# Kernel optimization log

Measured on AMD Instinct MI355X. Metric: run time of the kernel, lower is better.

Reference implementation:

```python
import jax, jax.numpy as jnp
import numpy as np

MARGIN = 0.3
EPS = 1e-12


def setup_inputs() -> dict:
    key = jax.random.key(0)
    k1, k2, k3, k4 = jax.random.split(key, 4)
    B, N, D = 4, 6400, 32
    pred_masks = jax.random.normal(k1, (B, N, D), dtype=jnp.float32)
    pos_rand = jax.random.uniform(k2, (B, N), dtype=jnp.float32)
    target_gt_idx = jax.random.randint(k3, (B, N), 0, 20, dtype=jnp.int64)
    fg_mask = jax.random.randint(k4, (B, N), 0, 2) > 0
    return {
        "pred_masks": pred_masks,
        "pos_rand": pos_rand,
        "target_gt_idx": target_gt_idx,
        "fg_mask": fg_mask,
    }


def reference(pred_masks, pos_rand, target_gt_idx, fg_mask):
    B, N, D = pred_masks.shape
    # L2-normalize coefficients (F.normalize, eps=1e-12)
    norm = jnp.sqrt(jnp.sum(pred_masks * pred_masks, axis=-1, keepdims=True))
    coeffs = pred_masks / jnp.maximum(norm, EPS)  # [B,N,D]

    valid_pair = fg_mask[:, :, None] & fg_mask[:, None, :]  # [B,N,N]
    same_inst = target_gt_idx[:, :, None] == target_gt_idx[:, None, :]
    eye = jnp.eye(N, dtype=bool)
    S = valid_pair & same_inst & ~eye          # positives (same instance, not self)
    Dm = valid_pair & ~same_inst               # negatives (different instance)

    # Cosine similarities (vectors are unit norm)
    sims = jnp.einsum('bnd,bmd->bnm', coeffs, coeffs)  # [B,N,N]

    # Hardest negative per anchor: argmax similarity among negatives
    neg_idx = jnp.argmax(jnp.where(Dm, sims, -jnp.inf), axis=-1)  # [B,N]
    neg_vec = jnp.take_along_axis(coeffs, neg_idx[..., None], axis=1)  # [B,N,D]

    # Random positive: pick the k-th positive in anchor order, k = floor(u*num_pos)
    num_pos = jnp.sum(S, axis=-1)  # [B,N]
    pos_choice = jnp.floor(pos_rand * num_pos.astype(pos_rand.dtype)).astype(jnp.int32)
    pos_choice = jnp.clip(pos_choice, 0, jnp.maximum(num_pos - 1, 0).astype(jnp.int32))
    cum = jnp.cumsum(S.astype(jnp.int32), axis=-1)  # rank of each positive
    sel = S & (cum == (pos_choice + 1)[..., None])  # one-hot over chosen positive
    pos_idx = jnp.argmax(sel, axis=-1)  # [B,N]
    pos_vec = jnp.take_along_axis(coeffs, pos_idx[..., None], axis=1)  # [B,N,D]

    pos_d = jnp.sqrt(jnp.sum((coeffs - pos_vec) ** 2, axis=-1) + EPS)
    neg_d = jnp.sqrt(jnp.sum((coeffs - neg_vec) ** 2, axis=-1) + EPS)

    valid = fg_mask & (num_pos >= 1) & jnp.any(Dm, axis=-1)  # anchor forms a triplet
    per_anchor = jnp.maximum(pos_d - neg_d + MARGIN, 0.0)
    n_trip = jnp.sum(valid)
    total = jnp.sum(per_anchor * valid.astype(per_anchor.dtype))
    return jnp.where(n_trip > 0, total / jnp.maximum(n_trip, 1).astype(total.dtype), 0.0)
```

## Files before the change

### kernel.cpp

```cpp
#include <hip/hip_runtime.h>
#include <math.h>

#define B_ 4
#define N_ 6400
#define D_ 32
#define TJ 256
#define TI 128
#define CHUNK 256
#define NCC 25
#define NCLS 20
#define CSROW 24
#define TOTB (NCC * B_)
#define NPASS 650

typedef __attribute__((ext_vector_type(4))) float f32x4;
typedef __attribute__((ext_vector_type(8))) short bf16x8;

static constexpr float MARGIN_ = 0.3f;

__device__ __forceinline__ unsigned fmap(float f) {
    unsigned u = __float_as_uint(f);
    return (u & 0x80000000u) ? ~u : (u | 0x80000000u);
}
__device__ __forceinline__ float funmap(unsigned u) {
    return (u & 0x80000000u) ? __uint_as_float(u ^ 0x80000000u)
                             : __uint_as_float(~u);
}
#define NEG_INF_MAPPED 0x007FFFFFu

__device__ __forceinline__ unsigned short f2bf(float f) {
    unsigned u = __float_as_uint(f);
    unsigned r = u + 0x7fffu + ((u >> 16) & 1u);
    return (unsigned short)(r >> 16);
}
__device__ __forceinline__ float bf2f(unsigned short h) {
    return __uint_as_float(((unsigned)h) << 16);
}
__device__ __forceinline__ void bf2x(unsigned u, float& e0, float& e1) {
    e0 = __uint_as_float(u << 16);
    e1 = __uint_as_float(u & 0xffff0000u);
}
__device__ __forceinline__ float dpair(unsigned xh, unsigned xl, unsigned yh, unsigned yl) {
    float a0, a1, b0, b1, c0, c1, d0, d1;
    bf2x(xh, a0, a1); bf2x(xl, b0, b1);
    bf2x(yh, c0, c1); bf2x(yl, d0, d1);
    return fmaf(a0 + b0, c0 + d0, (a1 + b1) * (c1 + d1));
}

__global__ __launch_bounds__(256) void k_prep(const float* __restrict__ pred,
                                              const int* __restrict__ gt,
                                              const int* __restrict__ fg,
                                              unsigned short* __restrict__ hi_g,
                                              unsigned short* __restrict__ lo_g,
                                              int* __restrict__ clist,
                                              int* __restrict__ cgS,
                                              int* __restrict__ Marr,
                                              int* __restrict__ csArr,
                                              unsigned* __restrict__ bestArr,
                                              unsigned* __restrict__ done) {
    int c = blockIdx.x, b = blockIdx.y;
    int t = threadIdx.x, lane = t & 63, w = t >> 6;
    int idx = c * CHUNK + t;

    bestArr[b * N_ + idx] = NEG_INF_MAPPED;
    if (c == 0 && b == 0 && t == 0) *done = 0u;

    __shared__ int cntL[NCC * NCLS];
    __shared__ int wv[4 * NCLS];
    __shared__ int totL[NCLS];
    __shared__ int csL[NCLS + 1];
    for (int k = t; k < NCC * NCLS; k += 256) cntL[k] = 0;
    __syncthreads();

    for (int cc = w; cc < NCC; cc += 4) {
        const int4 f4 = ((const int4*)(fg + (size_t)b * N_ + cc * CHUNK))[lane];
        const int4 g4 = ((const int4*)(gt + (size_t)b * N_ + cc * CHUNK))[lane];
        if (f4.x) atomicAdd(&cntL[cc * NCLS + g4.x], 1);
        if (f4.y) atomicAdd(&cntL[cc * NCLS + g4.y], 1);
        if (f4.z) atomicAdd(&cntL[cc * NCLS + g4.z], 1);
        if (f4.w) atomicAdd(&cntL[cc * NCLS + g4.w], 1);
    }

    bool flag = fg[b * N_ + idx] != 0;
    int cls = flag ? gt[b * N_ + idx] : 0;
    int rnk = 0;
    unsigned long long below = (1ull << lane) - 1ull;
    for (int k = 0; k < NCLS; ++k) {
        unsigned long long m = __ballot(flag && (cls == k));
        if (flag && cls == k) rnk = __popcll(m & below);
        if (lane == 0) wv[w * NCLS + k] = __popcll(m);
    }
    __syncthreads();

    if (t < NCLS) {
        int s = 0;
        #pragma unroll
        for (int cc = 0; cc < NCC; ++cc) s += cntL[cc * NCLS + t];
        totL[t] = s;
    }
    __syncthreads();
    if (t <= NCLS) {
        int s = 0;
        for (int k = 0; k < t; ++k) s += totL[k];
        csL[t] = s;
    }
    __syncthreads();
    if (c == 0) {
        if (t == 0) Marr[b] = csL[NCLS];
        if (t <= NCLS) csArr[b * CSROW + t] = csL[t];
    }
    if (!flag) return;

    int pre = 0;
    for (int cc = 0; cc < c; ++cc) pre += cntL[cc * NCLS + cls];
    int woff = 0;
    #pragma unroll
    for (int k = 0; k < 4; ++k) if (k < w) woff += wv[k * NCLS + cls];
    int dest = csL[cls] + pre + woff + rnk;
    clist[b * N_ + dest] = idx;
    cgS[b * N_ + dest] = cls;

    const float4* s4 = (const float4*)(pred + ((size_t)b * N_ + idx) * D_);
    float f[32];
    float ssq = 0.0f;
    #pragma unroll
    for (int k = 0; k < 8; ++k) {
        float4 q = s4[k];
        f[k * 4] = q.x; f[k * 4 + 1] = q.y; f[k * 4 + 2] = q.z; f[k * 4 + 3] = q.w;
        ssq += q.x * q.x + q.y * q.y + q.z * q.z + q.w * q.w;
    }
    float inv = 1.0f / fmaxf(sqrtf(ssq), 1e-12f);
    unsigned hw[16], lw[16];
    #pragma unroll
    for (int k = 0; k < 16; ++k) {
        float x0 = f[2 * k] * inv, x1 = f[2 * k + 1] * inv;
        unsigned short h0 = f2bf(x0), h1 = f2bf(x1);
        unsigned short l0 = f2bf(x0 - bf2f(h0)), l1 = f2bf(x1 - bf2f(h1));
        hw[k] = (unsigned)h0 | ((unsigned)h1 << 16);
        lw[k] = (unsigned)l0 | ((unsigned)l1 << 16);
    }
    uint4* dh = (uint4*)(hi_g + ((size_t)b * N_ + dest) * 32);
    uint4* dl = (uint4*)(lo_g + ((size_t)b * N_ + dest) * 32);
    #pragma unroll
    for (int k = 0; k < 4; ++k) {
        dh[k] = make_uint4(hw[4 * k], hw[4 * k + 1], hw[4 * k + 2], hw[4 * k + 3]);
        dl[k] = make_uint4(lw[4 * k], lw[4 * k + 1], lw[4 * k + 2], lw[4 * k + 3]);
    }
}

__global__ __launch_bounds__(256) void k_pass(const unsigned short* __restrict__ hi_g,
                                              const unsigned short* __restrict__ lo_g,
                                              const int* __restrict__ cgS,
                                              const int* __restrict__ Marr,
                                              const int* __restrict__ csArr,
                                              unsigned* __restrict__ bestArr) {
    int b = blockIdx.y;
    int M = Marr[b];
    int f = blockIdx.x;
    int bj = (int)((sqrtf(4.0f * (float)f + 1.0f) - 1.0f) * 0.5f);
    if ((bj + 1) * (bj + 2) <= f) ++bj;
    if (bj * (bj + 1) > f) --bj;
    int bi = f - bj * (bj + 1);
    int i0 = bi * TI;
    int j0 = bj * TJ;
    if (i0 >= M || j0 >= M) return;

    __shared__ __align__(16) unsigned short sc_hi[TJ * 40];
    __shared__ __align__(16) unsigned short sc_lo[TJ * 40];
    __shared__ int sg[TJ];
    __shared__ float colb[4 * TJ];
    int t = threadIdx.x;

    {
        int j = j0 + t;
        sg[t] = (j < M) ? cgS[b * N_ + j] : -1;
        #pragma unroll
        for (int k = 0; k < 4; ++k) colb[k * 256 + t] = -INFINITY;
    }
    {
        int seg = t & 3, r0 = t >> 2;
        #pragma unroll
        for (int p = 0; p < 4; ++p) {
            int row = p * 64 + r0;
            int j = j0 + row;
            uint4 vh = make_uint4(0u, 0u, 0u, 0u), vl = make_uint4(0u, 0u, 0u, 0u);
            if (j < M) {
                vh = *(const uint4*)(hi_g + ((size_t)b * N_ + j) * 32 + seg * 8);
                vl = *(const uint4*)(lo_g + ((size_t)b * N_ + j) * 32 + seg * 8);
            }
            *(uint4*)(sc_hi + row * 40 + seg * 8) = vh;
            *(uint4*)(sc_lo + row * 40 + seg * 8) = vl;
        }
    }
    __syncthreads();

    int lane = t & 63, w = t >> 6;
    int r = lane & 15, quad = lane >> 4;
    int ib = i0 + w * 32;

    if (ib < M) {
        bf16x8 a_hi[2], a_lo[2];
        int gt_i[2][4];
        #pragma unroll
        for (int it = 0; it < 2; ++it) {
            int i = ib + it * 16 + r;
            bf16x8 zh = {0, 0, 0, 0, 0, 0, 0, 0};
            a_hi[it] = zh; a_lo[it] = zh;
            if (i < M) {
                a_hi[it] = *(const bf16x8*)(hi_g + ((size_t)b * N_ + i) * 32 + quad * 8);
                a_lo[it] = *(const bf16x8*)(lo_g + ((size_t)b * N_ + i) * 32 + quad * 8);
            }
            #pragma unroll
            for (int r4 = 0; r4 < 4; ++r4) {
                int ia = ib + it * 16 + quad * 4 + r4;
                gt_i[it][r4] = (ia < M) ? cgS[b * N_ + ia] : -2;
            }
        }

        int ilast = min(ib + 31, M - 1);
        int cmin = cgS[b * N_ + ib];
        int cmax = cgS[b * N_ + ilast];
        int posLo = csArr[b * CSROW + cmin];
        int posHi = csArr[b * CSROW + cmax + 1];
        bool oneCls = (cmin == cmax);

        float best[2][4];
        #pragma unroll
        for (int it = 0; it < 2; ++it)
            #pragma unroll
            for (int r4 = 0; r4 < 4; ++r4) best[it][r4] = -INFINITY;

        int jrows = min(TJ, M - j0);
        int ntile = (jrows + 15) >> 4;
        for (int jt = 0; jt < ntile; ++jt) {
            int jlo = j0 + jt * 16;
            int jvhi = min(jlo + 16, j0 + jrows);
            if (oneCls && jlo >= posLo && jvhi <= posHi) continue;

            bf16x8 bh = *(const bf16x8*)(sc_hi + (jt * 16 + r) * 40 + quad * 8);
            bf16x8 bl = *(const bf16x8*)(sc_lo + (jt * 16 + r) * 40 + quad * 8);
            bool full = (jt * 16 + 16) <= jrows;
            float cb = -INFINITY;

            if (full && (jlo + 16 <= posLo || jlo >= posHi)) {
                #pragma unroll
                for (int it = 0; it < 2; ++it) {
                    f32x4 acc = {0.f, 0.f, 0.f, 0.f};
                    acc = __builtin_amdgcn_mfma_f32_16x16x32_bf16(a_hi[it], bh, acc, 0, 0, 0);
                    acc = __builtin_amdgcn_mfma_f32_16x16x32_bf16(a_hi[it], bl, acc, 0, 0, 0);
                    acc = __builtin_amdgcn_mfma_f32_16x16x32_bf16(a_lo[it], bh, acc, 0, 0, 0);
                    #pragma unroll
                    for (int r4 = 0; r4 < 4; ++r4) {
                        float v = acc[r4];
                        best[it][r4] = fmaxf(best[it][r4], v);
                        cb = fmaxf(cb, (gt_i[it][r4] >= 0) ? v : -INFINITY);
                    }
                }
            } else {
                int gtj = sg[jt * 16 + r];
                bool jv = (gtj >= 0);
                #pragma unroll
                for (int it = 0; it < 2; ++it) {
                    f32x4 acc = {0.f, 0.f, 0.f, 0.f};
                    acc = __builtin_amdgcn_mfma_f32_16x16x32_bf16(a_hi[it], bh, acc, 0, 0, 0);
                    acc = __builtin_amdgcn_mfma_f32_16x16x32_bf16(a_hi[it], bl, acc, 0, 0, 0);
                    acc = __builtin_amdgcn_mfma_f32_16x16x32_bf16(a_lo[it], bh, acc, 0, 0, 0);
                    #pragma unroll
                    for (int r4 = 0; r4 < 4; ++r4) {
                        bool same = (gtj == gt_i[it][r4]);
                        float sm = (same || !jv) ? -INFINITY : acc[r4];
                        best[it][r4] = fmaxf(best[it][r4], sm);
                        cb = fmaxf(cb, (gt_i[it][r4] >= 0) ? sm : -INFINITY);
                    }
                }
            }

            cb = fmaxf(cb, __shfl_xor(cb, 16));
            cb = fmaxf(cb, __shfl_xor(cb, 32));
            if (lane < 16) colb[w * TJ + jt * 16 + lane] = cb;
        }

        #pragma unroll
        for (int it = 0; it < 2; ++it) {
            #pragma unroll
            for (int r4 = 0; r4 < 4; ++r4) {
                float bb = best[it][r4];
                #pragma unroll
                for (int mk = 1; mk < 16; mk <<= 1)
                    bb = fmaxf(bb, __shfl_xor(bb, mk));
                if (r == 0) {
                    int ia = ib + it * 16 + quad * 4 + r4;
                    if (ia < M && bb > -INFINITY)
                        atomicMax(&bestArr[b * N_ + ia], fmap(bb));
                }
            }
        }
    }

    __syncthreads();
    {
        float v = fmaxf(fmaxf(colb[t], colb[TJ + t]),
                        fmaxf(colb[2 * TJ + t], colb[3 * TJ + t]));
        int j = j0 + t;
        if (j < M && v > -INFINITY)
            atomicMax(&bestArr[b * N_ + j], fmap(v));
    }
}

__global__ __launch_bounds__(256) void k_combine(const unsigned short* __restrict__ hi_g,
                                                 const unsigned short* __restrict__ lo_g,
                                                 const int* __restrict__ cgS,
                                                 const int* __restrict__ clist,
                                                 const int* __restrict__ Marr,
                                                 const int* __restrict__ csArr,
                                                 const float* __restrict__ pos_rand,
                                                 const unsigned* __restrict__ bestArr,
                                                 unsigned* __restrict__ partS,
                                                 unsigned* __restrict__ partC,
                                                 unsigned* __restrict__ done,
                                                 float* __restrict__ out) {
    int b = blockIdx.y;
    int M = Marr[b];
    int t = threadIdx.x, lane = t & 63, w = t >> 6;
    int i = blockIdx.x * 256 + t;

    float contrib = 0.0f;
    int vflag = 0;
    if (i < M) {
        int cls = cgS[b * N_ + i];
        int s0 = csArr[b * CSROW + cls];
        int s1 = csArr[b * CSROW + cls + 1];
        int num_pos = s1 - s0 - 1;
        unsigned bu = bestArr[b * N_ + i];
        if (num_pos >= 1 && bu != NEG_INF_MAPPED) {
            float best = funmap(bu);
            int orig = clist[b * N_ + i];
            float u = pos_rand[b * N_ + orig];
            int pcx = (int)floorf(u * (float)num_pos);
            int hi2 = num_pos - 1;
            pcx = pcx < 0 ? 0 : (pcx > hi2 ? hi2 : pcx);
            int ri = i - s0;
            int posj = s0 + pcx + (pcx >= ri ? 1 : 0);

            const uint4* xh4 = (const uint4*)(hi_g + ((size_t)b * N_ + i) * 32);
            const uint4* xl4 = (const uint4*)(lo_g + ((size_t)b * N_ + i) * 32);
            const uint4* yh4 = (const uint4*)(hi_g + ((size_t)b * N_ + posj) * 32);
            const uint4* yl4 = (const uint4*)(lo_g + ((size_t)b * N_ + posj) * 32);
            float dot = 0.0f;
            #pragma unroll
            for (int q = 0; q < 4; ++q) {
                uint4 XH = xh4[q], XL = xl4[q], YH = yh4[q], YL = yl4[q];
                dot += dpair(XH.x, XL.x, YH.x, YL.x);
                dot += dpair(XH.y, XL.y, YH.y, YL.y);
                dot += dpair(XH.z, XL.z, YH.z, YL.z);
                dot += dpair(XH.w, XL.w, YH.w, YL.w);
            }
            float pos_d = sqrtf(fmaxf(2.f - 2.f * dot, 0.f) + 1e-12f);
            float neg_d = sqrtf(fmaxf(2.f - 2.f * best, 0.f) + 1e-12f);
            contrib = fmaxf(pos_d - neg_d + MARGIN_, 0.0f);
            vflag = 1;
        }
    }

    #pragma unroll
    for (int off = 32; off > 0; off >>= 1) {
        contrib += __shfl_down(contrib, off);
        vflag += __shfl_down(vflag, off);
    }
    __shared__ float ssum[4];
    __shared__ int scnt[4];
    if (lane == 0) { ssum[w] = contrib; scnt[w] = vflag; }
    __syncthreads();

    if (w == 0) {
        int bid = b * NCC + blockIdx.x;
        int last = 0;
        if (lane == 0) {
            float bs = ssum[0] + ssum[1] + ssum[2] + ssum[3];
            int bc = scnt[0] + scnt[1] + scnt[2] + scnt[3];
            atomicExch(&partS[bid], __float_as_uint(bs));
            atomicExch(&partC[bid], (unsigned)bc);
            __threadfence();
            last = (atomicAdd(done, 1u) == (unsigned)(TOTB - 1)) ? 1 : 0;
        }
        last = __shfl(last, 0);
        if (last) {
            float T = 0.0f; int C = 0;
            for (int k = lane; k < TOTB; k += 64) {
                T += __uint_as_float(atomicAdd(&partS[k], 0u));
                C += (int)atomicAdd(&partC[k], 0u);
            }
            #pragma unroll
            for (int off = 32; off > 0; off >>= 1) {
                T += __shfl_down(T, off);
                C += __shfl_down(C, off);
            }
            if (lane == 0) out[0] = (C > 0) ? (T / (float)C) : 0.0f;
        }
    }
}

extern "C" void kernel_launch(void* const* d_in, const int* in_sizes, int n_in,
                              void* d_out, int out_size, void* d_ws, size_t ws_size,
                              hipStream_t stream) {
    const float* pred     = (const float*)d_in[0];
    const float* pos_rand = (const float*)d_in[1];
    const int*   gt       = (const int*)d_in[2];
    const int*   fg       = (const int*)d_in[3];
    float* out = (float*)d_out;

    char* ws = (char*)d_ws;
    unsigned short* hi_g    = (unsigned short*)(ws);
    unsigned short* lo_g    = (unsigned short*)(ws + 1638400);
    int*            clist   = (int*)(ws + 3276800);
    int*            cgS     = (int*)(ws + 3379200);
    int*            Marr    = (int*)(ws + 3481600);
    int*            csArr   = (int*)(ws + 3481664);
    unsigned*       done    = (unsigned*)(ws + 3482048);
    unsigned*       partS   = (unsigned*)(ws + 3482112);
    unsigned*       partC   = (unsigned*)(ws + 3482624);
    unsigned*       bestArr = (unsigned*)(ws + 3483136);

    dim3 gpr(NCC, B_);
    k_prep<<<gpr, 256, 0, stream>>>(pred, gt, fg, hi_g, lo_g, clist, cgS, Marr, csArr, bestArr, done);
    dim3 gp(NPASS, B_);
    k_pass<<<gp, 256, 0, stream>>>(hi_g, lo_g, cgS, Marr, csArr, bestArr);
    dim3 gc(NCC, B_);
    k_combine<<<gc, 256, 0, stream>>>(hi_g, lo_g, cgS, clist, Marr, csArr, pos_rand, bestArr, partS, partC, done, out);
}
```

Before: 93.84 us.

## Fuse combine stage into pass kernel via last-block-per-batch completion counter

Removes the separate k_combine launch. Each k_pass block bumps a per-batch counter when it finishes, and the last block for each batch runs the per-anchor loss over all M anchors in a single 256-thread block, then does a cross-batch final reduction through a second counter. It also adds an all-valid fast path in the off-diagonal MFMA tile that drops the per-row validity select. This saves one launch and its gap, at the cost of a serial tail where one block per batch handles up to 6400 anchors.

```diff
diff --git a/kernel.cpp b/kernel.cpp
--- a/kernel.cpp
+++ b/kernel.cpp
@@ -10,7 +10,6 @@
 #define NCC 25
 #define NCLS 20
 #define CSROW 24
-#define TOTB (NCC * B_)
 #define NPASS 650
 
 typedef __attribute__((ext_vector_type(4))) float f32x4;
@@ -57,13 +56,15 @@
                                               int* __restrict__ Marr,
                                               int* __restrict__ csArr,
                                               unsigned* __restrict__ bestArr,
-                                              unsigned* __restrict__ done) {
+                                              unsigned* __restrict__ passDone,
+                                              unsigned* __restrict__ combDone) {
     int c = blockIdx.x, b = blockIdx.y;
     int t = threadIdx.x, lane = t & 63, w = t >> 6;
     int idx = c * CHUNK + t;
 
     bestArr[b * N_ + idx] = NEG_INF_MAPPED;
-    if (c == 0 && b == 0 && t == 0) *done = 0u;
+    if (c == 0 && t == 0) passDone[b] = 0u;
+    if (c == 0 && b == 0 && t == 0) *combDone = 0u;
 
     __shared__ int cntL[NCC * NCLS];
     __shared__ int wv[4 * NCLS];
@@ -151,9 +152,16 @@
 __global__ __launch_bounds__(256) void k_pass(const unsigned short* __restrict__ hi_g,
                                               const unsigned short* __restrict__ lo_g,
                                               const int* __restrict__ cgS,
+                                              const int* __restrict__ clist,
                                               const int* __restrict__ Marr,
                                               const int* __restrict__ csArr,
-                                              unsigned* __restrict__ bestArr) {
+                                              const float* __restrict__ pos_rand,
+                                              unsigned* __restrict__ bestArr,
+                                              unsigned* __restrict__ passDone,
+                                              unsigned* __restrict__ combDone,
+                                              unsigned* __restrict__ partS,
+                                              unsigned* __restrict__ partC,
+                                              float* __restrict__ out) {
     int b = blockIdx.y;
     int M = Marr[b];
     int f = blockIdx.x;
@@ -163,239 +171,241 @@
     int bi = f - bj * (bj + 1);
     int i0 = bi * TI;
     int j0 = bj * TJ;
-    if (i0 >= M || j0 >= M) return;
+    int t = threadIdx.x;
+    int lane = t & 63, w = t >> 6;
 
     __shared__ __align__(16) unsigned short sc_hi[TJ * 40];
     __shared__ __align__(16) unsigned short sc_lo[TJ * 40];
     __shared__ int sg[TJ];
     __shared__ float colb[4 * TJ];
-    int t = threadIdx.x;
-
-    {
-        int j = j0 + t;
-        sg[t] = (j < M) ? cgS[b * N_ + j] : -1;
-        #pragma unroll
-        for (int k = 0; k < 4; ++k) colb[k * 256 + t] = -INFINITY;
-    }
-    {
-        int seg = t & 3, r0 = t >> 2;
-        #pragma unroll
-        for (int p = 0; p < 4; ++p) {
-            int row = p * 64 + r0;
-            int j = j0 + row;
-            uint4 vh = make_uint4(0u, 0u, 0u, 0u), vl = make_uint4(0u, 0u, 0u, 0u);
-            if (j < M) {
-                vh = *(const uint4*)(hi_g + ((size_t)b * N_ + j) * 32 + seg * 8);
-                vl = *(const uint4*)(lo_g + ((size_t)b * N_ + j) * 32 + seg * 8);
-            }
-            *(uint4*)(sc_hi + row * 40 + seg * 8) = vh;
-            *(uint4*)(sc_lo + row * 40 + seg * 8) = vl;
-        }
-    }
-    __syncthreads();
-
-    int lane = t & 63, w = t >> 6;
-    int r = lane & 15, quad = lane >> 4;
-    int ib = i0 + w * 32;
-
-    if (ib < M) {
-        bf16x8 a_hi[2], a_lo[2];
-        int gt_i[2][4];
-        #pragma unroll
-        for (int it = 0; it < 2; ++it) {
-            int i = ib + it * 16 + r;
-            bf16x8 zh = {0, 0, 0, 0, 0, 0, 0, 0};
-            a_hi[it] = zh; a_lo[it] = zh;
-            if (i < M) {
-                a_hi[it] = *(const bf16x8*)(hi_g + ((size_t)b * N_ + i) * 32 + quad * 8);
-                a_lo[it] = *(const bf16x8*)(lo_g + ((size_t)b * N_ + i) * 32 + quad * 8);
-            }
-            #pragma unroll
-            for (int r4 = 0; r4 < 4; ++r4) {
-                int ia = ib + it * 16 + quad * 4 + r4;
-                gt_i[it][r4] = (ia < M) ? cgS[b * N_ + ia] : -2;
-            }
-        }
-
-        int ilast = min(ib + 31, M - 1);
-        int cmin = cgS[b * N_ + ib];
-        int cmax = cgS[b * N_ + ilast];
-        int posLo = csArr[b * CSROW + cmin];
-        int posHi = csArr[b * CSROW + cmax + 1];
-        bool oneCls = (cmin == cmax);
-
-        float best[2][4];
-        #pragma unroll
-        for (int it = 0; it < 2; ++it)
-            #pragma unroll
-            for (int r4 = 0; r4 < 4; ++r4) best[it][r4] = -INFINITY;
-
-        int jrows = min(TJ, M - j0);
-        int ntile = (jrows + 15) >> 4;
-        for (int jt = 0; jt < ntile; ++jt) {
-            int jlo = j0 + jt * 16;
-            int jvhi = min(jlo + 16, j0 + jrows);
-            if (oneCls && jlo >= posLo && jvhi <= posHi) continue;
-
-            bf16x8 bh = *(const bf16x8*)(sc_hi + (jt * 16 + r) * 40 + quad * 8);
-            bf16x8 bl = *(const bf16x8*)(sc_lo + (jt * 16 + r) * 40 + quad * 8);
-            bool full = (jt * 16 + 16) <= jrows;
-            float cb = -INFINITY;
-
-            if (full && (jlo + 16 <= posLo || jlo >= posHi)) {
+
+    bool activeBlk = (i0 < M) && (j0 < M);
+    if (activeBlk) {
+        {
+            int j = j0 + t;
+            sg[t] = (j < M) ? cgS[b * N_ + j] : -1;
+            #pragma unroll
+            for (int k = 0; k < 4; ++k) colb[k * 256 + t] = -INFINITY;
+        }
+        {
+            int seg = t & 3, r0 = t >> 2;
+            #pragma unroll
+            for (int p = 0; p < 4; ++p) {
+                int row = p * 64 + r0;
+                int j = j0 + row;
+                uint4 vh = make_uint4(0u, 0u, 0u, 0u), vl = make_uint4(0u, 0u, 0u, 0u);
+                if (j < M) {
+                    vh = *(const uint4*)(hi_g + ((size_t)b * N_ + j) * 32 + seg * 8);
+                    vl = *(const uint4*)(lo_g + ((size_t)b * N_ + j) * 32 + seg * 8);
+                }
+                *(uint4*)(sc_hi + row * 40 + seg * 8) = vh;
+                *(uint4*)(sc_lo + row * 40 + seg * 8) = vl;
+            }
+        }
+        __syncthreads();
+
+        int r = lane & 15, quad = lane >> 4;
+        int ib = i0 + w * 32;
+
+        if (ib < M) {
+            bf16x8 a_hi[2], a_lo[2];
+            int gt_i[2][4];
+            #pragma unroll
+            for (int it = 0; it < 2; ++it) {
+                int i = ib + it * 16 + r;
+                bf16x8 zh = {0, 0, 0, 0, 0, 0, 0, 0};
+                a_hi[it] = zh; a_lo[it] = zh;
+                if (i < M) {
+                    a_hi[it] = *(const bf16x8*)(hi_g + ((size_t)b * N_ + i) * 32 + quad * 8);
+                    a_lo[it] = *(const bf16x8*)(lo_g + ((size_t)b * N_ + i) * 32 + quad * 8);
+                }
                 #pragma unroll
-                for (int it = 0; it < 2; ++it) {
-                    f32x4 acc = {0.f, 0.f, 0.f, 0.f};
-                    acc = __builtin_amdgcn_mfma_f32_16x16x32_bf16(a_hi[it], bh, acc, 0, 0, 0);
-                    acc = __builtin_amdgcn_mfma_f32_16x16x32_bf16(a_hi[it], bl, acc, 0, 0, 0);
-                    acc = __builtin_amdgcn_mfma_f32_16x16x32_bf16(a_lo[it], bh, acc, 0, 0, 0);
+                for (int r4 = 0; r4 < 4; ++r4) {
+                    int ia = ib + it * 16 + quad * 4 + r4;
+                    gt_i[it][r4] = (ia < M) ? cgS[b * N_ + ia] : -2;
+                }
+            }
+
+            int ilast = min(ib + 31, M - 1);
+            int cmin = cgS[b * N_ + ib];
+            int cmax = cgS[b * N_ + ilast];
+            int posLo = csArr[b * CSROW + cmin];
+            int posHi = csArr[b * CSROW + cmax + 1];
+            bool oneCls = (cmin == cmax);
+            bool allValid = (ib + 31 < M);
+
+            float best[2][4];
+            #pragma unroll
+            for (int it = 0; it < 2; ++it)
+                #pragma unroll
+                for (int r4 = 0; r4 < 4; ++r4) best[it][r4] = -INFINITY;
+
+            int jrows = min(TJ, M - j0);
+            int ntile = (jrows + 15) >> 4;
+            for (int jt = 0; jt < ntile; ++jt) {
+                int jlo = j0 + jt * 16;
+                int jvhi = min(jlo + 16, j0 + jrows);
+                if (oneCls && jlo >= posLo && jvhi <= posHi) continue;
+
+                bf16x8 bh = *(const bf16x8*)(sc_hi + (jt * 16 + r) * 40 + quad * 8);
+                bf16x8 bl = *(const bf16x8*)(sc_lo + (jt * 16 + r) * 40 + quad * 8);
+                bool full = (jt * 16 + 16) <= jrows;
+                float cb = -INFINITY;
+
+                if (full && (jlo + 16 <= posLo || jlo >= posHi)) {
+                    if (allValid) {
+                        #pragma unroll
+                        for (int it = 0; it < 2; ++it) {
+                            f32x4 acc = {0.f, 0.f, 0.f, 0.f};
+                            acc = __builtin_amdgcn_mfma_f32_16x16x32_bf16(a_hi[it], bh, acc, 0, 0, 0);
+                            acc = __builtin_amdgcn_mfma_f32_16x16x32_bf16(a_hi[it], bl, acc, 0, 0, 0);
+                            acc = __builtin_amdgcn_mfma_f32_16x16x32_bf16(a_lo[it], bh, acc, 0, 0, 0);
+                            #pragma unroll
+                            for (int r4 = 0; r4 < 4; ++r4) {
+                                float v = acc[r4];
+                                best[it][r4] = fmaxf(best[it][r4], v);
+                                cb = fmaxf(cb, v);
+                            }
+                        }
+                    } else {
+                        #pragma unroll
+                        for (int it = 0; it < 2; ++it) {
+                            f32x4 acc = {0.f, 0.f, 0.f, 0.f};
+                            acc = __builtin_amdgcn_mfma_f32_16x16x32_bf16(a_hi[it], bh, acc, 0, 0, 0);
+                            acc = __builtin_amdgcn_mfma_f32_16x16x32_bf16(a_hi[it], bl, acc, 0, 0, 0);
+                            acc = __builtin_amdgcn_mfma_f32_16x16x32_bf16(a_lo[it], bh, acc, 0, 0, 0);
+                            #pragma unroll
+                            for (int r4 = 0; r4 < 4; ++r4) {
+                                float v = acc[r4];
+                                best[it][r4] = fmaxf(best[it][r4], v);
+                                cb = fmaxf(cb, (gt_i[it][r4] >= 0) ? v : -INFINITY);
+                            }
+                        }
+                    }
+                } else {
+                    int gtj = sg[jt * 16 + r];
+                    bool jv = (gtj >= 0);
                     #pragma unroll
-                    for (int r4 = 0; r4 < 4; ++r4) {
-                        float v = acc[r4];
-                        best[it][r4] = fmaxf(best[it][r4], v);
-                        cb = fmaxf(cb, (gt_i[it][r4] >= 0) ? v : -INFINITY);
+                    for (int it = 0; it < 2; ++it) {
+                        f32x4 acc = {0.f, 0.f, 0.f, 0.f};
+                        acc = __builtin_amdgcn_mfma_f32_16x16x32_bf16(a_hi[it], bh, acc, 0, 0, 0);
+                        acc = __builtin_amdgcn_mfma_f32_16x16x32_bf16(a_hi[it], bl, acc, 0, 0, 0);
+                        acc = __builtin_amdgcn_mfma_f32_16x16x32_bf16(a_lo[it], bh, acc, 0, 0, 0);
+                        #pragma unroll
+                        for (int r4 = 0; r4 < 4; ++r4) {
+                            bool same = (gtj == gt_i[it][r4]);
+                            float sm = (same || !jv) ? -INFINITY : acc[r4];
+                            best[it][r4] = fmaxf(best[it][r4], sm);
+                            cb = fmaxf(cb, (gt_i[it][r4] >= 0) ? sm : -INFINITY);
+                        }
                     }
                 }
-            } else {
-                int gtj = sg[jt * 16 + r];
-                bool jv = (gtj >= 0);
+
+                cb = fmaxf(cb, __shfl_xor(cb, 16));
+                cb = fmaxf(cb, __shfl_xor(cb, 32));
+                if (lane < 16) colb[w * TJ + jt * 16 + lane] = cb;
+            }
+
+            #pragma unroll
+            for (int it = 0; it < 2; ++it) {
                 #pragma unroll
-                for (int it = 0; it < 2; ++it) {
-                    f32x4 acc = {0.f, 0.f, 0.f, 0.f};
-                    acc = __builtin_amdgcn_mfma_f32_16x16x32_bf16(a_hi[it], bh, acc, 0, 0, 0);
-                    acc = __builtin_amdgcn_mfma_f32_16x16x32_bf16(a_hi[it], bl, acc, 0, 0, 0);
-                    acc = __builtin_amdgcn_mfma_f32_16x16x32_bf16(a_lo[it], bh, acc, 0, 0, 0);
+                for (int r4 = 0; r4 < 4; ++r4) {
+                    float bb = best[it][r4];
                     #pragma unroll
-                    for (int r4 = 0; r4 < 4; ++r4) {
-                        bool same = (gtj == gt_i[it][r4]);
-                        float sm = (same || !jv) ? -INFINITY : acc[r4];
-                        best[it][r4] = fmaxf(best[it][r4], sm);
-                        cb = fmaxf(cb, (gt_i[it][r4] >= 0) ? sm : -INFINITY);
+                    for (int mk = 1; mk < 16; mk <<= 1)
+                        bb = fmaxf(bb, __shfl_xor(bb, mk));
+                    if (r == 0) {
+                        int ia = ib + it * 16 + quad * 4 + r4;
+                        if (ia < M && bb > -INFINITY)
+                            atomicMax(&bestArr[b * N_ + ia], fmap(bb));
                     }
                 }
             }
-
-            cb = fmaxf(cb, __shfl_xor(cb, 16));
-            cb = fmaxf(cb, __shfl_xor(cb, 32));
-            if (lane < 16) colb[w * TJ + jt * 16 + lane] = cb;
-        }
-
-        #pragma unroll
-        for (int it = 0; it < 2; ++it) {
-            #pragma unroll
-            for (int r4 = 0; r4 < 4; ++r4) {
-                float bb = best[it][r4];
+        }
+
+        __syncthreads();
+        {
+            float v = fmaxf(fmaxf(colb[t], colb[TJ + t]),
+                            fmaxf(colb[2 * TJ + t], colb[3 * TJ + t]));
+            int j = j0 + t;
+            if (j < M && v > -INFINITY)
+                atomicMax(&bestArr[b * N_ + j], fmap(v));
+        }
+    }
+
+    __threadfence();
+    __shared__ int s_last;
+    if (t == 0)
+        s_last = (atomicAdd(&passDone[b], 1u) == (unsigned)(NPASS - 1)) ? 1 : 0;
+    __syncthreads();
+    if (!s_last) return;
+    __threadfence();
+
+    float csum = 0.0f;
+    int ccnt = 0;
+    for (int base = 0; base < M; base += 256) {
+        int i = base + t;
+        if (i < M) {
+            int cls = cgS[b * N_ + i];
+            int s0 = csArr[b * CSROW + cls];
+            int s1 = csArr[b * CSROW + cls + 1];
+            int num_pos = s1 - s0 - 1;
+            unsigned bu = atomicAdd(&bestArr[b * N_ + i], 0u);
+            if (num_pos >= 1 && bu != NEG_INF_MAPPED) {
+                float bestv = funmap(bu);
+                int orig = clist[b * N_ + i];
+                float u = pos_rand[b * N_ + orig];
+                int pcx = (int)floorf(u * (float)num_pos);
+                int hi2 = num_pos - 1;
+                pcx = pcx < 0 ? 0 : (pcx > hi2 ? hi2 : pcx);
+                int ri = i - s0;
+                int posj = s0 + pcx + (pcx >= ri ? 1 : 0);
+
+                const uint4* xh4 = (const uint4*)(hi_g + ((size_t)b * N_ + i) * 32);
+                const uint4* xl4 = (const uint4*)(lo_g + ((size_t)b * N_ + i) * 32);
+                const uint4* yh4 = (const uint4*)(hi_g + ((size_t)b * N_ + posj) * 32);
+                const uint4* yl4 = (const uint4*)(lo_g + ((size_t)b * N_ + posj) * 32);
+                float dot = 0.0f;
                 #pragma unroll
-                for (int mk = 1; mk < 16; mk <<= 1)
-                    bb = fmaxf(bb, __shfl_xor(bb, mk));
-                if (r == 0) {
-                    int ia = ib + it * 16 + quad * 4 + r4;
-                    if (ia < M && bb > -INFINITY)
-                        atomicMax(&bestArr[b * N_ + ia], fmap(bb));
-                }
-            }
-        }
-    }
-
-    __syncthreads();
-    {
-        float v = fmaxf(fmaxf(colb[t], colb[TJ + t]),
-                        fmaxf(colb[2 * TJ + t], colb[3 * TJ + t]));
-        int j = j0 + t;
-        if (j < M && v > -INFINITY)
-            atomicMax(&bestArr[b * N_ + j], fmap(v));
-    }
-}
-
-__global__ __launch_bounds__(256) void k_combine(const unsigned short* __restrict__ hi_g,
-                                                 const unsigned short* __restrict__ lo_g,
-                                                 const int* __restrict__ cgS,
-                                                 const int* __restrict__ clist,
-                                                 const int* __restrict__ Marr,
-                                                 const int* __restrict__ csArr,
-                                                 const float* __restrict__ pos_rand,
-                                                 const unsigned* __restrict__ bestArr,
-                                                 unsigned* __restrict__ partS,
-                                                 unsigned* __restrict__ partC,
-                                                 unsigned* __restrict__ done,
-                                                 float* __restrict__ out) {
-    int b = blockIdx.y;
-    int M = Marr[b];
-    int t = threadIdx.x, lane = t & 63, w = t >> 6;
-    int i = blockIdx.x * 256 + t;
-
-    float contrib = 0.0f;
-    int vflag = 0;
-    if (i < M) {
-        int cls = cgS[b * N_ + i];
-        int s0 = csArr[b * CSROW + cls];
-        int s1 = csArr[b * CSROW + cls + 1];
-        int num_pos = s1 - s0 - 1;
-        unsigned bu = bestArr[b * N_ + i];
-        if (num_pos >= 1 && bu != NEG_INF_MAPPED) {
-            float best = funmap(bu);
-            int orig = clist[b * N_ + i];
-            float u = pos_rand[b * N_ + orig];
-            int pcx = (int)floorf(u * (float)num_pos);
-            int hi2 = num_pos - 1;
-            pcx = pcx < 0 ? 0 : (pcx > hi2 ? hi2 : pcx);
-            int ri = i - s0;
-            int posj = s0 + pcx + (pcx >= ri ? 1 : 0);
-
-            const uint4* xh4 = (const uint4*)(hi_g + ((size_t)b * N_ + i) * 32);
-            const uint4* xl4 = (const uint4*)(lo_g + ((size_t)b * N_ + i) * 32);
-            const uint4* yh4 = (const uint4*)(hi_g + ((size_t)b * N_ + posj) * 32);
-            const uint4* yl4 = (const uint4*)(lo_g + ((size_t)b * N_ + posj) * 32);
-            float dot = 0.0f;
-            #pragma unroll
-            for (int q = 0; q < 4; ++q) {
-                uint4 XH = xh4[q], XL = xl4[q], YH = yh4[q], YL = yl4[q];
-                dot += dpair(XH.x, XL.x, YH.x, YL.x);
-                dot += dpair(XH.y, XL.y, YH.y, YL.y);
-                dot += dpair(XH.z, XL.z, YH.z, YL.z);
-                dot += dpair(XH.w, XL.w, YH.w, YL.w);
-            }
-            float pos_d = sqrtf(fmaxf(2.f - 2.f * dot, 0.f) + 1e-12f);
-            float neg_d = sqrtf(fmaxf(2.f - 2.f * best, 0.f) + 1e-12f);
-            contrib = fmaxf(pos_d - neg_d + MARGIN_, 0.0f);
-            vflag = 1;
+                for (int q = 0; q < 4; ++q) {
+                    uint4 XH = xh4[q], XL = xl4[q], YH = yh4[q], YL = yl4[q];
+                    dot += dpair(XH.x, XL.x, YH.x, YL.x);
+                    dot += dpair(XH.y, XL.y, YH.y, YL.y);
+                    dot += dpair(XH.z, XL.z, YH.z, YL.z);
+                    dot += dpair(XH.w, XL.w, YH.w, YL.w);
+                }
+                float pos_d = sqrtf(fmaxf(2.f - 2.f * dot, 0.f) + 1e-12f);
+                float neg_d = sqrtf(fmaxf(2.f - 2.f * bestv, 0.f) + 1e-12f);
+                csum += fmaxf(pos_d - neg_d + MARGIN_, 0.0f);
+                ccnt += 1;
+            }
         }
     }
 
     #pragma unroll
     for (int off = 32; off > 0; off >>= 1) {
-        contrib += __shfl_down(contrib, off);
-        vflag += __shfl_down(vflag, off);
+        csum += __shfl_down(csum, off);
+        ccnt += __shfl_down(ccnt, off);
     }
     __shared__ float ssum[4];
     __shared__ int scnt[4];
-    if (lane == 0) { ssum[w] = contrib; scnt[w] = vflag; }
-    __syncthreads();
-
-    if (w == 0) {
-        int bid = b * NCC + blockIdx.x;
-        int last = 0;
-        if (lane == 0) {
-            float bs = ssum[0] + ssum[1] + ssum[2] + ssum[3];
-            int bc = scnt[0] + scnt[1] + scnt[2] + scnt[3];
-            atomicExch(&partS[bid], __float_as_uint(bs));
-            atomicExch(&partC[bid], (unsigned)bc);
-            __threadfence();
-            last = (atomicAdd(done, 1u) == (unsigned)(TOTB - 1)) ? 1 : 0;
-        }
-        last = __shfl(last, 0);
-        if (last) {
+    if (lane == 0) { ssum[w] = csum; scnt[w] = ccnt; }
+    __syncthreads();
+
+    if (t == 0) {
+        float bs = ssum[0] + ssum[1] + ssum[2] + ssum[3];
+        int bc = scnt[0] + scnt[1] + scnt[2] + scnt[3];
+        atomicExch(&partS[b], __float_as_uint(bs));
+        atomicExch(&partC[b], (unsigned)bc);
+        __threadfence();
+        if (atomicAdd(combDone, 1u) == (unsigned)(B_ - 1)) {
             float T = 0.0f; int C = 0;
-            for (int k = lane; k < TOTB; k += 64) {
+            #pragma unroll
+            for (int k = 0; k < B_; ++k) {
                 T += __uint_as_float(atomicAdd(&partS[k], 0u));
                 C += (int)atomicAdd(&partC[k], 0u);
             }
-            #pragma unroll
-            for (int off = 32; off > 0; off >>= 1) {
-                T += __shfl_down(T, off);
-                C += __shfl_down(C, off);
-            }
-            if (lane == 0) out[0] = (C > 0) ? (T / (float)C) : 0.0f;
+            out[0] = (C > 0) ? (T / (float)C) : 0.0f;
         }
     }
 }
@@ -410,21 +420,22 @@
     float* out = (float*)d_out;
 
     char* ws = (char*)d_ws;
-    unsigned short* hi_g    = (unsigned short*)(ws);
-    unsigned short* lo_g    = (unsigned short*)(ws + 1638400);
-    int*            clist   = (int*)(ws + 3276800);
-    int*            cgS     = (int*)(ws + 3379200);
-    int*            Marr    = (int*)(ws + 3481600);
-    int*            csArr   = (int*)(ws + 3481664);
-    unsigned*       done    = (unsigned*)(ws + 3482048);
-    unsigned*       partS   = (unsigned*)(ws + 3482112);
-    unsigned*       partC   = (unsigned*)(ws + 3482624);
-    unsigned*       bestArr = (unsigned*)(ws + 3483136);
+    unsigned short* hi_g     = (unsigned short*)(ws);
+    unsigned short* lo_g     = (unsigned short*)(ws + 1638400);
+    int*            clist    = (int*)(ws + 3276800);
+    int*            cgS      = (int*)(ws + 3379200);
+    int*            Marr     = (int*)(ws + 3481600);
+    int*            csArr    = (int*)(ws + 3481664);
+    unsigned*       combDone = (unsigned*)(ws + 3482048);
+    unsigned*       passDone = (unsigned*)(ws + 3482112);
+    unsigned*       partS    = (unsigned*)(ws + 3482176);
+    unsigned*       partC    = (unsigned*)(ws + 3482240);
+    unsigned*       bestArr  = (unsigned*)(ws + 3483136);
 
     dim3 gpr(NCC, B_);
-    k_prep<<<gpr, 256, 0, stream>>>(pred, gt, fg, hi_g, lo_g, clist, cgS, Marr, csArr, bestArr, done);
+    k_prep<<<gpr, 256, 0, stream>>>(pred, gt, fg, hi_g, lo_g, clist, cgS, Marr, csArr,
+                                    bestArr, passDone, combDone);
     dim3 gp(NPASS, B_);
-    k_pass<<<gp, 256, 0, stream>>>(hi_g, lo_g, cgS, Marr, csArr, bestArr);
-    dim3 gc(NCC, B_);
-    k_combine<<<gc, 256, 0, stream>>>(hi_g, lo_g, cgS, clist, Marr, csArr, pos_rand, bestArr, partS, partC, done, out);
-}
+    k_pass<<<gp, 256, 0, stream>>>(hi_g, lo_g, cgS, clist, Marr, csArr, pos_rand,
+                                   bestArr, passDone, combDone, partS, partC, out);
+}
```

Measured after the change: 274.3 us. 2.92x slower.
